# Performance work log

Measured on AMD Instinct MI355X. Metric: run time of the kernel, lower is better.

The kernel has to match this reference:

```python
import jax, jax.numpy as jnp
import numpy as np

B, S, D = 2, 2048, 1024
H, KV, HD = 16, 4, 64          # query heads, kv heads, head_dim
ROT = 32                        # partial rotary dim
G = H // KV                     # GQA group size
SCALE = HD ** -0.5


def _rotate_half(x):
    x1, x2 = x[..., : x.shape[-1] // 2], x[..., x.shape[-1] // 2 :]
    return jnp.concatenate((-x2, x1), axis=-1)


def setup_inputs() -> dict:
    key = jax.random.key(0)
    ks = jax.random.split(key, 8)
    hidden_states = jax.random.normal(ks[0], (B, S, D), dtype=jnp.float32)
    # real rotary tables: inv_freq over ROT//2 frequencies, duplicated halves
    inv_freq = 1.0 / (10000.0 ** (jnp.arange(0, ROT, 2, dtype=jnp.float32) / ROT))
    ang = jnp.arange(S, dtype=jnp.float32)[:, None] * inv_freq[None, :]  # [S, ROT/2]
    emb = jnp.concatenate([ang, ang], axis=-1)                           # [S, ROT]
    cos = jnp.broadcast_to(jnp.cos(emb)[None], (B, S, ROT))
    sin = jnp.broadcast_to(jnp.sin(emb)[None], (B, S, ROT))
    sd = lambda fan_in: 1.0 / np.sqrt(fan_in)
    q_w = jax.random.normal(ks[1], (D, H * HD), jnp.float32) * sd(D)
    q_b = jax.random.normal(ks[2], (H * HD,), jnp.float32) * 0.02
    k_w = jax.random.normal(ks[3], (D, KV * HD), jnp.float32) * sd(D)
    v_w = jax.random.normal(ks[4], (D, KV * HD), jnp.float32) * sd(D)
    v_b = jax.random.normal(ks[5], (KV * HD,), jnp.float32) * 0.02
    o_w = jax.random.normal(ks[6], (H * HD, D), jnp.float32) * sd(H * HD)
    o_b = jax.random.normal(ks[7], (D,), jnp.float32) * 0.02
    return {"hidden_states": hidden_states, "cos": cos, "sin": sin,
            "q_w": q_w, "q_b": q_b, "k_w": k_w, "v_w": v_w, "v_b": v_b,
            "o_w": o_w, "o_b": o_b}


def reference(hidden_states, cos, sin, q_w, q_b, k_w, v_w, v_b, o_w, o_b):
    x = hidden_states
    # projections -> [B, heads, S, HD]
    q = (x @ q_w + q_b).reshape(B, S, H, HD).transpose(0, 2, 1, 3)
    k = (x @ k_w).reshape(B, S, KV, HD).transpose(0, 2, 1, 3)
    v = (x @ v_w + v_b).reshape(B, S, KV, HD).transpose(0, 2, 1, 3)
    # partial RoPE; cos/sin broadcast over head dim
    c = cos[:, None, :, :]
    s = sin[:, None, :, :]
    q_rot, q_pass = q[..., :ROT], q[..., ROT:]
    k_rot, k_pass = k[..., :ROT], k[..., ROT:]
    q = jnp.concatenate([q_rot * c + _rotate_half(q_rot) * s, q_pass], axis=-1)
    k = jnp.concatenate([k_rot * c + _rotate_half(k_rot) * s, k_pass], axis=-1)
    # GQA without materializing repeated K/V: group queries per kv head
    qg = q.reshape(B, KV, G, S, HD)
    scores = jnp.einsum("bkgsd,bktd->bkgst", qg, k) * SCALE  # [B,KV,G,S,S]
    probs = jax.nn.softmax(scores, axis=-1)
    out = jnp.einsum("bkgst,bktd->bkgsd", probs, v)          # [B,KV,G,S,HD]
    out = out.reshape(B, H, S, HD).transpose(0, 2, 1, 3).reshape(B, S, H * HD)
    attn_output = out @ o_w + o_b
    attn_weights = probs.reshape(B, H, S, S)
    return attn_output, attn_weights
```

## Files before the change

### kernel.cpp

```cpp
#include <hip/hip_runtime.h>
#include <hip/hip_bf16.h>

typedef _Float16 f16;
typedef _Float16 f16x8 __attribute__((ext_vector_type(8)));
typedef _Float16 f16x4 __attribute__((ext_vector_type(4)));
typedef float f32x4 __attribute__((ext_vector_type(4)));

#define MFMA_F16(a, b, c) __builtin_amdgcn_mfma_f32_16x16x32_f16((a), (b), (c), 0, 0, 0)

static constexpr int S_TOK = 2048;
static constexpr int N_HEAD = 16;
static constexpr int N_KV = 4;
static constexpr int HD = 64;
static constexpr float SCL2E = 0.125f * 1.4426950408889634f;

static constexpr size_t OFF_X16 = 0;
static constexpr size_t OFF_QW = 4194304;
static constexpr size_t OFF_KW = OFF_QW + 1048576;
static constexpr size_t OFF_VW = OFF_KW + 262144;
static constexpr size_t OFF_OW = OFF_VW + 262144;
static constexpr size_t OFF_QS = OFF_OW + 1048576;
static constexpr size_t OFF_KS = OFF_QS + 4194304;
static constexpr size_t OFF_VS = OFF_KS + 1048576;
static constexpr size_t OFF_OS = OFF_VS + 1048576;
static constexpr size_t CVT_TOTAL = OFF_OW + 1048576;

__global__ __launch_bounds__(256) void k_cvt(
    const float* __restrict__ x, const float* __restrict__ qw,
    const float* __restrict__ kw, const float* __restrict__ vw,
    const float* __restrict__ ow, f16* __restrict__ dst) {
  size_t i = ((size_t)blockIdx.x * 256 + threadIdx.x) * 4;
  if (i >= CVT_TOTAL) return;
  const float* src;
  size_t off;
  if (i < OFF_QW) { src = x; off = i; }
  else if (i < OFF_KW) { src = qw; off = i - OFF_QW; }
  else if (i < OFF_VW) { src = kw; off = i - OFF_KW; }
  else if (i < OFF_OW) { src = vw; off = i - OFF_VW; }
  else { src = ow; off = i - OFF_OW; }
  float4 v = *(const float4*)(src + off);
  *(f16x4*)(dst + i) = f16x4{(f16)v.x, (f16)v.y, (f16)v.z, (f16)v.w};
}

__global__ __launch_bounds__(256) void k_qkv(
    const f16* __restrict__ x, const float* __restrict__ cosp,
    const float* __restrict__ sinp, const f16* __restrict__ q_w,
    const float* __restrict__ q_b, const f16* __restrict__ k_w,
    const f16* __restrict__ v_w, const float* __restrict__ v_b,
    f16* __restrict__ q_ws, f16* __restrict__ k_ws, f16* __restrict__ v_ws) {
  __shared__ f16 wb[64][72];
  const int tid = threadIdx.x;
  const int wave = tid >> 6, lane = tid & 63;
  const int l16 = lane & 15, g = lane >> 4;
  const int m0 = blockIdx.x * 64;
  const int n0 = blockIdx.y * 64;

  const f16* W;
  int ldW, nloc, mode;
  if (n0 < 1024) { W = q_w; ldW = 1024; nloc = n0; mode = 0; }
  else if (n0 < 1280) { W = k_w; ldW = 256; nloc = n0 - 1024; mode = 1; }
  else { W = v_w; ldW = 256; nloc = n0 - 1280; mode = 2; }

  f32x4 acc[4] = {};
  const int kk = (tid >> 4) * 4;
  const int nn = (tid & 15) * 4;

  for (int k0 = 0; k0 < 1024; k0 += 64) {
    const f16* wp = W + (size_t)(k0 + kk) * ldW + nloc + nn;
    f16x4 w0 = *(const f16x4*)(wp);
    f16x4 w1 = *(const f16x4*)(wp + ldW);
    f16x4 w2 = *(const f16x4*)(wp + 2 * ldW);
    f16x4 w3 = *(const f16x4*)(wp + 3 * ldW);
    __syncthreads();
    *(f16x4*)&wb[nn + 0][kk] = f16x4{w0[0], w1[0], w2[0], w3[0]};
    *(f16x4*)&wb[nn + 1][kk] = f16x4{w0[1], w1[1], w2[1], w3[1]};
    *(f16x4*)&wb[nn + 2][kk] = f16x4{w0[2], w1[2], w2[2], w3[2]};
    *(f16x4*)&wb[nn + 3][kk] = f16x4{w0[3], w1[3], w2[3], w3[3]};
    __syncthreads();
    const f16* xp = x + (size_t)(m0 + wave * 16 + l16) * 1024 + k0 + g * 8;
#pragma unroll
    for (int ks = 0; ks < 2; ++ks) {
      f16x8 af = *(const f16x8*)(xp + ks * 32);
#pragma unroll
      for (int n = 0; n < 4; ++n) {
        f16x8 bf = *(const f16x8*)&wb[n * 16 + l16][ks * 32 + g * 8];
        acc[n] = MFMA_F16(af, bf, acc[n]);
      }
    }
  }

  if (mode == 0) {
#pragma unroll
    for (int n = 0; n < 4; ++n) {
      float bsc = q_b[n0 + n * 16 + l16];
#pragma unroll
      for (int r = 0; r < 4; ++r) acc[n][r] += bsc;
    }
  } else if (mode == 2) {
#pragma unroll
    for (int n = 0; n < 4; ++n) {
      float bsc = v_b[nloc + n * 16 + l16];
#pragma unroll
      for (int r = 0; r < 4; ++r) acc[n][r] += bsc;
    }
  }
  if (mode < 2) {
#pragma unroll
    for (int r = 0; r < 4; ++r) {
      int row = m0 + wave * 16 + g * 4 + r;
      int bb = row >> 11, ss = row & 2047;
      float c = cosp[((size_t)bb * S_TOK + ss) * 32 + l16];
      float sn = sinp[((size_t)bb * S_TOK + ss) * 32 + l16];
      float v0 = acc[0][r], v1 = acc[1][r];
      acc[0][r] = v0 * c - v1 * sn;
      acc[1][r] = v1 * c + v0 * sn;
    }
  }
#pragma unroll
  for (int n = 0; n < 4; ++n) {
#pragma unroll
    for (int r = 0; r < 4; ++r) {
      int row = m0 + wave * 16 + g * 4 + r;
      int bb = row >> 11, ss = row & 2047;
      f16 val = (f16)acc[n][r];
      if (mode == 0) {
        int col = n0 + n * 16 + l16;
        int h = col >> 6, hd = col & 63;
        q_ws[(((size_t)bb * N_HEAD + h) * S_TOK + ss) * HD + hd] = val;
      } else {
        int col = nloc + n * 16 + l16;
        int kh = col >> 6, hd = col & 63;
        if (mode == 1)
          k_ws[(((size_t)bb * N_KV + kh) * S_TOK + ss) * HD + hd] = val;
        else
          v_ws[(((size_t)bb * N_KV + kh) * HD + hd) * S_TOK + ss] = val;
      }
    }
  }
}

__global__ __launch_bounds__(256, 3) void k_attn(
    const f16* __restrict__ q_ws, const f16* __restrict__ k_ws,
    const f16* __restrict__ v_ws, f16* __restrict__ o_ws,
    float* __restrict__ probs) {
  __shared__ f16 plds_all[4][32][72];
  __shared__ float lpart[2][2][32];
  __shared__ float osum[2][32][68];
  const int tid = threadIdx.x;
  const int wave = tid >> 6, lane = tid & 63;
  const int pairi = wave >> 1, half = wave & 1;
  const int l16 = lane & 15, g = lane >> 4;
  const int bid = blockIdx.x;
  const int combo = bid & 7, local = bid >> 3;
  const int b = combo >> 2, kvh = combo & 3;
  const int h = kvh * 4 + (local >> 5);
  const int rt = local & 31;
  const int head = b * N_HEAD + h;
  const int qrow0 = rt * 64 + pairi * 32;

  const f16* qb = q_ws + ((size_t)head * S_TOK + qrow0) * HD;
  const f16* kb = k_ws + (size_t)(b * N_KV + kvh) * S_TOK * HD;
  const f16* vb = v_ws + (size_t)(b * N_KV + kvh) * HD * S_TOK;
  float* pout = probs + (size_t)head * S_TOK * S_TOK + (size_t)qrow0 * S_TOK;
  f16(*plds)[72] = plds_all[wave];

  f16x8 qf[2][2];
#pragma unroll
  for (int mf = 0; mf < 2; ++mf)
#pragma unroll
    for (int ks = 0; ks < 2; ++ks)
      qf[mf][ks] = *(const f16x8*)(qb + (mf * 16 + l16) * HD + ks * 32 + g * 8);

  const int kt0 = half * 16, kt1 = kt0 + 16;

  float lsum[2][4] = {};
  for (int kt = kt0; kt < kt1; ++kt) {
    const f16* kp = kb + (size_t)kt * 64 * HD;
#pragma unroll
    for (int n = 0; n < 4; ++n) {
      f16x8 k0f = *(const f16x8*)(kp + (n * 16 + l16) * HD + g * 8);
      f16x8 k1f = *(const f16x8*)(kp + (n * 16 + l16) * HD + 32 + g * 8);
#pragma unroll
      for (int mf = 0; mf < 2; ++mf) {
        f32x4 s = {};
        s = MFMA_F16(qf[mf][0], k0f, s);
        s = MFMA_F16(qf[mf][1], k1f, s);
#pragma unroll
        for (int r = 0; r < 4; ++r) lsum[mf][r] += exp2f(s[r] * SCL2E);
      }
    }
  }
#pragma unroll
  for (int mf = 0; mf < 2; ++mf)
#pragma unroll
    for (int r = 0; r < 4; ++r) {
      float v = lsum[mf][r];
      v += __shfl_xor(v, 1, 64);
      v += __shfl_xor(v, 2, 64);
      v += __shfl_xor(v, 4, 64);
      v += __shfl_xor(v, 8, 64);
      lsum[mf][r] = v;
    }
  if (l16 == 0) {
#pragma unroll
    for (int mf = 0; mf < 2; ++mf)
#pragma unroll
      for (int r = 0; r < 4; ++r)
        lpart[pairi][half][mf * 16 + g * 4 + r] = lsum[mf][r];
  }
  __syncthreads();
  float linv[2][4];
#pragma unroll
  for (int mf = 0; mf < 2; ++mf)
#pragma unroll
    for (int r = 0; r < 4; ++r) {
      int row = mf * 16 + g * 4 + r;
      linv[mf][r] = 1.0f / (lpart[pairi][0][row] + lpart[pairi][1][row]);
    }

  f32x4 oacc[2][4] = {};
  const int orow = lane >> 4, oq = lane & 15;
  for (int kt = kt0; kt < kt1; ++kt) {
    const f16* kp = kb + (size_t)kt * 64 * HD;
#pragma unroll
    for (int n = 0; n < 4; ++n) {
      f16x8 k0f = *(const f16x8*)(kp + (n * 16 + l16) * HD + g * 8);
      f16x8 k1f = *(const f16x8*)(kp + (n * 16 + l16) * HD + 32 + g * 8);
#pragma unroll
      for (int mf = 0; mf < 2; ++mf) {
        f32x4 s = {};
        s = MFMA_F16(qf[mf][0], k0f, s);
        s = MFMA_F16(qf[mf][1], k1f, s);
#pragma unroll
        for (int r = 0; r < 4; ++r) {
          float p = exp2f(s[r] * SCL2E) * linv[mf][r];
          plds[mf * 16 + g * 4 + r][n * 16 + l16] = (f16)p;
        }
      }
    }
    asm volatile("s_waitcnt lgkmcnt(0)" ::: "memory");
    f16x8 pa[2][2];
#pragma unroll
    for (int mf = 0; mf < 2; ++mf)
#pragma unroll
      for (int ks = 0; ks < 2; ++ks)
        pa[mf][ks] = *(const f16x8*)&plds[mf * 16 + l16][ks * 32 + g * 8];
#pragma unroll
    for (int nh = 0; nh < 4; ++nh) {
      const f16* vp = vb + (size_t)(nh * 16 + l16) * S_TOK + kt * 64;
      f16x8 v0f = *(const f16x8*)(vp + g * 8);
      f16x8 v1f = *(const f16x8*)(vp + 32 + g * 8);
#pragma unroll
      for (int mf = 0; mf < 2; ++mf) {
        oacc[mf][nh] = MFMA_F16(pa[mf][0], v0f, oacc[mf][nh]);
        oacc[mf][nh] = MFMA_F16(pa[mf][1], v1f, oacc[mf][nh]);
      }
    }
#pragma unroll
    for (int it = 0; it < 8; ++it) {
      int rr = it * 4 + orow;
      f16x4 pv = *(const f16x4*)&plds[rr][oq * 4];
      f32x4 ov = {(float)pv[0], (float)pv[1], (float)pv[2], (float)pv[3]};
      __builtin_nontemporal_store(
          ov, (f32x4*)(pout + (size_t)rr * S_TOK + kt * 64 + oq * 4));
    }
    asm volatile("" ::: "memory");
  }

  if (half == 1) {
#pragma unroll
    for (int mf = 0; mf < 2; ++mf)
#pragma unroll
      for (int nh = 0; nh < 4; ++nh)
#pragma unroll
        for (int r = 0; r < 4; ++r)
          osum[pairi][mf * 16 + g * 4 + r][nh * 16 + l16] = oacc[mf][nh][r];
  }
  __syncthreads();
  if (half == 0) {
#pragma unroll
    for (int mf = 0; mf < 2; ++mf)
#pragma unroll
      for (int nh = 0; nh < 4; ++nh)
#pragma unroll
        for (int r = 0; r < 4; ++r) {
          int row = mf * 16 + g * 4 + r;
          float v = oacc[mf][nh][r] + osum[pairi][row][nh * 16 + l16];
          o_ws[((size_t)b * S_TOK + qrow0 + row) * 1024 + h * HD + nh * 16 +
               l16] = (f16)v;
        }
  }
}

__global__ __launch_bounds__(256) void k_oproj(
    const f16* __restrict__ a, const f16* __restrict__ o_w,
    const float* __restrict__ o_b, float* __restrict__ out) {
  __shared__ f16 wb[64][72];
  const int tid = threadIdx.x;
  const int wave = tid >> 6, lane = tid & 63;
  const int l16 = lane & 15, g = lane >> 4;
  const int m0 = blockIdx.x * 64, n0 = blockIdx.y * 64;
  f32x4 acc[4] = {};
  const int kk = (tid >> 4) * 4, nn = (tid & 15) * 4;
  for (int k0 = 0; k0 < 1024; k0 += 64) {
    const f16* wp = o_w + (size_t)(k0 + kk) * 1024 + n0 + nn;
    f16x4 w0 = *(const f16x4*)(wp);
    f16x4 w1 = *(const f16x4*)(wp + 1024);
    f16x4 w2 = *(const f16x4*)(wp + 2048);
    f16x4 w3 = *(const f16x4*)(wp + 3072);
    __syncthreads();
    *(f16x4*)&wb[nn + 0][kk] = f16x4{w0[0], w1[0], w2[0], w3[0]};
    *(f16x4*)&wb[nn + 1][kk] = f16x4{w0[1], w1[1], w2[1], w3[1]};
    *(f16x4*)&wb[nn + 2][kk] = f16x4{w0[2], w1[2], w2[2], w3[2]};
    *(f16x4*)&wb[nn + 3][kk] = f16x4{w0[3], w1[3], w2[3], w3[3]};
    __syncthreads();
    const f16* ap = a + (size_t)(m0 + wave * 16 + l16) * 1024 + k0 + g * 8;
#pragma unroll
    for (int ks = 0; ks < 2; ++ks) {
      f16x8 af = *(const f16x8*)(ap + ks * 32);
#pragma unroll
      for (int n = 0; n < 4; ++n) {
        f16x8 bf = *(const f16x8*)&wb[n * 16 + l16][ks * 32 + g * 8];
        acc[n] = MFMA_F16(af, bf, acc[n]);
      }
    }
  }
#pragma unroll
  for (int n = 0; n < 4; ++n) {
    float bsc = o_b[n0 + n * 16 + l16];
#pragma unroll
    for (int r = 0; r < 4; ++r) {
      int row = m0 + wave * 16 + g * 4 + r;
      out[(size_t)row * 1024 + n0 + n * 16 + l16] = acc[n][r] + bsc;
    }
  }
}

extern "C" void kernel_launch(void* const* d_in, const int* in_sizes, int n_in,
                              void* d_out, int out_size, void* d_ws,
                              size_t ws_size, hipStream_t stream) {
  (void)in_sizes; (void)n_in; (void)out_size; (void)ws_size;
  const float* x    = (const float*)d_in[0];
  const float* cosp = (const float*)d_in[1];
  const float* sinp = (const float*)d_in[2];
  const float* q_w  = (const float*)d_in[3];
  const float* q_b  = (const float*)d_in[4];
  const float* k_w  = (const float*)d_in[5];
  const float* v_w  = (const float*)d_in[6];
  const float* v_b  = (const float*)d_in[7];
  const float* o_w  = (const float*)d_in[8];
  const float* o_b  = (const float*)d_in[9];

  f16* ws = (f16*)d_ws;
  f16* x16  = ws + OFF_X16;
  f16* qw16 = ws + OFF_QW;
  f16* kw16 = ws + OFF_KW;
  f16* vw16 = ws + OFF_VW;
  f16* ow16 = ws + OFF_OW;
  f16* q_ws = ws + OFF_QS;
  f16* k_ws = ws + OFF_KS;
  f16* v_ws = ws + OFF_VS;
  f16* o_ws = ws + OFF_OS;
  float* out = (float*)d_out;
  float* probs = out + 4194304;

  k_cvt<<<dim3((CVT_TOTAL / 4 + 255) / 256), 256, 0, stream>>>(
      x, q_w, k_w, v_w, o_w, ws);
  k_qkv<<<dim3(64, 24), 256, 0, stream>>>(x16, cosp, sinp, qw16, q_b, kw16,
                                          vw16, v_b, q_ws, k_ws, v_ws);
  k_attn<<<dim3(1024), 256, 0, stream>>>(q_ws, k_ws, v_ws, o_ws, probs);
  k_oproj<<<dim3(64, 16), 256, 0, stream>>>(o_ws, ow16, o_b, out);
}
```

Measured before the change: 304.6 us.

## Split softmax row-sum pass into separate kernel writing partial sums to workspace

Moves the first pass of the two-pass attention (computing exp row sums over keys) out of k_attn into a new k_lsum kernel. k_lsum uses 2048 blocks with one 16-row tile per wave, and it stores two half-range partial sums per row in the x16 workspace region, which is no longer needed after the QKV projection. k_attn then reads the partial sums, drops its shared-memory reduction and __syncthreads, and computes only the normalized probabilities and PV. This aims for more parallelism and lower register pressure in each pass, at the cost of an extra kernel launch, a global round trip for the sums, and a second read of Q and K.

```diff
diff --git a/kernel.cpp b/kernel.cpp
--- a/kernel.cpp
+++ b/kernel.cpp
@@ -139,12 +139,54 @@
   }
 }
 
+__global__ __launch_bounds__(256) void k_lsum(
+    const f16* __restrict__ q_ws, const f16* __restrict__ k_ws,
+    float* __restrict__ lsum_ws) {
+  const int tid = threadIdx.x;
+  const int wave = tid >> 6, lane = tid & 63;
+  const int l16 = lane & 15, g = lane >> 4;
+  const int bid = blockIdx.x;
+  const int combo = bid & 7, local = bid >> 3;
+  const int b = combo >> 2, kvh = combo & 3;
+  const int hg = local >> 6;
+  const int rem = local & 63;
+  const int qt = rem >> 1, half = rem & 1;
+  const int head = b * N_HEAD + kvh * 4 + hg;
+  const int qrow0 = qt * 64 + wave * 16;
+
+  const f16* qb = q_ws + ((size_t)head * S_TOK + qrow0) * HD;
+  const f16* kb = k_ws + (size_t)(b * N_KV + kvh) * S_TOK * HD;
+
+  f16x8 qf[2];
+  qf[0] = *(const f16x8*)(qb + l16 * HD + g * 8);
+  qf[1] = *(const f16x8*)(qb + l16 * HD + 32 + g * 8);
+
+  float lsum = 0.0f;
+  const int kt0 = half * 16, kt1 = kt0 + 16;
+  for (int kt = kt0; kt < kt1; ++kt) {
+    const f16* kp = kb + (size_t)kt * 64 * HD;
+#pragma unroll
+    for (int n = 0; n < 4; ++n) {
+      f16x8 k0f = *(const f16x8*)(kp + (n * 16 + l16) * HD + g * 8);
+      f16x8 k1f = *(const f16x8*)(kp + (n * 16 + l16) * HD + 32 + g * 8);
+      f32x4 s = {};
+      s = MFMA_F16(k0f, qf[0], s);
+      s = MFMA_F16(k1f, qf[1], s);
+      lsum += exp2f(s[0] * SCL2E) + exp2f(s[1] * SCL2E) +
+              exp2f(s[2] * SCL2E) + exp2f(s[3] * SCL2E);
+    }
+  }
+  lsum += __shfl_xor(lsum, 16, 64);
+  lsum += __shfl_xor(lsum, 32, 64);
+  if (lane < 16)
+    lsum_ws[((size_t)head * S_TOK + qrow0 + l16) * 2 + half] = lsum;
+}
+
 __global__ __launch_bounds__(256, 3) void k_attn(
     const f16* __restrict__ q_ws, const f16* __restrict__ k_ws,
-    const f16* __restrict__ v_ws, f16* __restrict__ o_ws,
-    float* __restrict__ probs) {
+    const f16* __restrict__ v_ws, const float* __restrict__ lsum_ws,
+    f16* __restrict__ o_ws, float* __restrict__ probs) {
   __shared__ f16 plds_all[4][32][72];
-  __shared__ float lpart[2][2][32];
   __shared__ float osum[2][32][68];
   const int tid = threadIdx.x;
   const int wave = tid >> 6, lane = tid & 63;
@@ -171,52 +213,16 @@
     for (int ks = 0; ks < 2; ++ks)
       qf[mf][ks] = *(const f16x8*)(qb + (mf * 16 + l16) * HD + ks * 32 + g * 8);
 
+  float linv[2][4];
+#pragma unroll
+  for (int mf = 0; mf < 2; ++mf)
+#pragma unroll
+    for (int r = 0; r < 4; ++r) {
+      size_t base = ((size_t)head * S_TOK + qrow0 + mf * 16 + g * 4 + r) * 2;
+      linv[mf][r] = 1.0f / (lsum_ws[base] + lsum_ws[base + 1]);
+    }
+
   const int kt0 = half * 16, kt1 = kt0 + 16;
-
-  float lsum[2][4] = {};
-  for (int kt = kt0; kt < kt1; ++kt) {
-    const f16* kp = kb + (size_t)kt * 64 * HD;
-#pragma unroll
-    for (int n = 0; n < 4; ++n) {
-      f16x8 k0f = *(const f16x8*)(kp + (n * 16 + l16) * HD + g * 8);
-      f16x8 k1f = *(const f16x8*)(kp + (n * 16 + l16) * HD + 32 + g * 8);
-#pragma unroll
-      for (int mf = 0; mf < 2; ++mf) {
-        f32x4 s = {};
-        s = MFMA_F16(qf[mf][0], k0f, s);
-        s = MFMA_F16(qf[mf][1], k1f, s);
-#pragma unroll
-        for (int r = 0; r < 4; ++r) lsum[mf][r] += exp2f(s[r] * SCL2E);
-      }
-    }
-  }
-#pragma unroll
-  for (int mf = 0; mf < 2; ++mf)
-#pragma unroll
-    for (int r = 0; r < 4; ++r) {
-      float v = lsum[mf][r];
-      v += __shfl_xor(v, 1, 64);
-      v += __shfl_xor(v, 2, 64);
-      v += __shfl_xor(v, 4, 64);
-      v += __shfl_xor(v, 8, 64);
-      lsum[mf][r] = v;
-    }
-  if (l16 == 0) {
-#pragma unroll
-    for (int mf = 0; mf < 2; ++mf)
-#pragma unroll
-      for (int r = 0; r < 4; ++r)
-        lpart[pairi][half][mf * 16 + g * 4 + r] = lsum[mf][r];
-  }
-  __syncthreads();
-  float linv[2][4];
-#pragma unroll
-  for (int mf = 0; mf < 2; ++mf)
-#pragma unroll
-    for (int r = 0; r < 4; ++r) {
-      int row = mf * 16 + g * 4 + r;
-      linv[mf][r] = 1.0f / (lpart[pairi][0][row] + lpart[pairi][1][row]);
-    }
 
   f32x4 oacc[2][4] = {};
   const int orow = lane >> 4, oq = lane & 15;
@@ -361,6 +367,7 @@
   f16* k_ws = ws + OFF_KS;
   f16* v_ws = ws + OFF_VS;
   f16* o_ws = ws + OFF_OS;
+  float* lsum_ws = (float*)(ws + OFF_X16);
   float* out = (float*)d_out;
   float* probs = out + 4194304;
 
@@ -368,6 +375,8 @@
       x, q_w, k_w, v_w, o_w, ws);
   k_qkv<<<dim3(64, 24), 256, 0, stream>>>(x16, cosp, sinp, qw16, q_b, kw16,
                                           vw16, v_b, q_ws, k_ws, v_ws);
-  k_attn<<<dim3(1024), 256, 0, stream>>>(q_ws, k_ws, v_ws, o_ws, probs);
+  k_lsum<<<dim3(2048), 256, 0, stream>>>(q_ws, k_ws, lsum_ws);
+  k_attn<<<dim3(1024), 256, 0, stream>>>(q_ws, k_ws, v_ws, lsum_ws, o_ws,
+                                         probs);
   k_oproj<<<dim3(64, 16), 256, 0, stream>>>(o_ws, ow16, o_b, out);
 }
```

Measured after the change: 372.5 us. 22.3% more time.

## Use 128x128 LDS-tiled GEMMs with 2x2 wave layout for QKV and output projections

Applied to the files above, without the earlier changes.

The QKV and output-projection GEMMs now use 128x128 block tiles. Both the activation tile and the weight tile are staged in shared memory, and each wave computes a 64x64 sub-tile (4x4 MFMAs), where before A was read straight from global memory per wave. This raises arithmetic intensity and reuse of both operands, cutting global traffic per MFMA. In exchange there are fewer blocks (384 and 256), which may underfill the GPU's compute units, and register and LDS use per block goes up.

```diff
diff --git a/kernel.cpp b/kernel.cpp
--- a/kernel.cpp
+++ b/kernel.cpp
@@ -48,95 +48,127 @@
     const float* __restrict__ q_b, const f16* __restrict__ k_w,
     const f16* __restrict__ v_w, const float* __restrict__ v_b,
     f16* __restrict__ q_ws, f16* __restrict__ k_ws, f16* __restrict__ v_ws) {
-  __shared__ f16 wb[64][72];
+  __shared__ f16 at[128][72];
+  __shared__ f16 bt[128][72];
   const int tid = threadIdx.x;
   const int wave = tid >> 6, lane = tid & 63;
   const int l16 = lane & 15, g = lane >> 4;
-  const int m0 = blockIdx.x * 64;
-  const int n0 = blockIdx.y * 64;
+  const int wm = wave >> 1, wn = wave & 1;
+  const int m0 = blockIdx.x * 128;
+  const int n0 = blockIdx.y * 128;
 
   const f16* W;
-  int ldW, nloc, mode;
-  if (n0 < 1024) { W = q_w; ldW = 1024; nloc = n0; mode = 0; }
-  else if (n0 < 1280) { W = k_w; ldW = 256; nloc = n0 - 1024; mode = 1; }
-  else { W = v_w; ldW = 256; nloc = n0 - 1280; mode = 2; }
-
-  f32x4 acc[4] = {};
-  const int kk = (tid >> 4) * 4;
-  const int nn = (tid & 15) * 4;
+  int ldW, nbase;
+  if (n0 < 1024) { W = q_w; ldW = 1024; nbase = n0; }
+  else if (n0 < 1280) { W = k_w; ldW = 256; nbase = n0 - 1024; }
+  else { W = v_w; ldW = 256; nbase = n0 - 1280; }
+
+  f32x4 acc[4][4] = {};
+  const int arow = tid >> 3, asub = tid & 7;
+  const int bkr = (tid >> 4) * 4, bnc = (tid & 15) * 4;
 
   for (int k0 = 0; k0 < 1024; k0 += 64) {
-    const f16* wp = W + (size_t)(k0 + kk) * ldW + nloc + nn;
-    f16x4 w0 = *(const f16x4*)(wp);
-    f16x4 w1 = *(const f16x4*)(wp + ldW);
-    f16x4 w2 = *(const f16x4*)(wp + 2 * ldW);
-    f16x4 w3 = *(const f16x4*)(wp + 3 * ldW);
+    f16x8 av[4];
+#pragma unroll
+    for (int it = 0; it < 4; ++it)
+      av[it] = *(const f16x8*)(x + (size_t)(m0 + it * 32 + arow) * 1024 + k0 +
+                               asub * 8);
+    f16x4 bv[2][4];
+#pragma unroll
+    for (int it = 0; it < 2; ++it)
+#pragma unroll
+      for (int kk = 0; kk < 4; ++kk)
+        bv[it][kk] = *(const f16x4*)(W + (size_t)(k0 + bkr + kk) * ldW + nbase +
+                                     it * 64 + bnc);
     __syncthreads();
-    *(f16x4*)&wb[nn + 0][kk] = f16x4{w0[0], w1[0], w2[0], w3[0]};
-    *(f16x4*)&wb[nn + 1][kk] = f16x4{w0[1], w1[1], w2[1], w3[1]};
-    *(f16x4*)&wb[nn + 2][kk] = f16x4{w0[2], w1[2], w2[2], w3[2]};
-    *(f16x4*)&wb[nn + 3][kk] = f16x4{w0[3], w1[3], w2[3], w3[3]};
+#pragma unroll
+    for (int it = 0; it < 4; ++it)
+      *(f16x8*)&at[it * 32 + arow][asub * 8] = av[it];
+#pragma unroll
+    for (int it = 0; it < 2; ++it)
+#pragma unroll
+      for (int i = 0; i < 4; ++i)
+        *(f16x4*)&bt[it * 64 + bnc + i][bkr] =
+            f16x4{bv[it][0][i], bv[it][1][i], bv[it][2][i], bv[it][3][i]};
     __syncthreads();
-    const f16* xp = x + (size_t)(m0 + wave * 16 + l16) * 1024 + k0 + g * 8;
 #pragma unroll
     for (int ks = 0; ks < 2; ++ks) {
-      f16x8 af = *(const f16x8*)(xp + ks * 32);
-#pragma unroll
-      for (int n = 0; n < 4; ++n) {
-        f16x8 bf = *(const f16x8*)&wb[n * 16 + l16][ks * 32 + g * 8];
-        acc[n] = MFMA_F16(af, bf, acc[n]);
-      }
-    }
-  }
+      f16x8 af[4], bf[4];
+#pragma unroll
+      for (int mi = 0; mi < 4; ++mi)
+        af[mi] = *(const f16x8*)&at[wm * 64 + mi * 16 + l16][ks * 32 + g * 8];
+#pragma unroll
+      for (int ni = 0; ni < 4; ++ni)
+        bf[ni] = *(const f16x8*)&bt[wn * 64 + ni * 16 + l16][ks * 32 + g * 8];
+#pragma unroll
+      for (int mi = 0; mi < 4; ++mi)
+#pragma unroll
+        for (int ni = 0; ni < 4; ++ni)
+          acc[mi][ni] = MFMA_F16(af[mi], bf[ni], acc[mi][ni]);
+    }
+  }
+
+  const int gc0 = n0 + wn * 64;
+  int mode, nloc;
+  if (gc0 < 1024) { mode = 0; nloc = gc0; }
+  else if (gc0 < 1280) { mode = 1; nloc = gc0 - 1024; }
+  else { mode = 2; nloc = gc0 - 1280; }
 
   if (mode == 0) {
 #pragma unroll
-    for (int n = 0; n < 4; ++n) {
-      float bsc = q_b[n0 + n * 16 + l16];
-#pragma unroll
-      for (int r = 0; r < 4; ++r) acc[n][r] += bsc;
+    for (int ni = 0; ni < 4; ++ni) {
+      float bsc = q_b[gc0 + ni * 16 + l16];
+#pragma unroll
+      for (int mi = 0; mi < 4; ++mi)
+#pragma unroll
+        for (int r = 0; r < 4; ++r) acc[mi][ni][r] += bsc;
     }
   } else if (mode == 2) {
 #pragma unroll
-    for (int n = 0; n < 4; ++n) {
-      float bsc = v_b[nloc + n * 16 + l16];
-#pragma unroll
-      for (int r = 0; r < 4; ++r) acc[n][r] += bsc;
+    for (int ni = 0; ni < 4; ++ni) {
+      float bsc = v_b[nloc + ni * 16 + l16];
+#pragma unroll
+      for (int mi = 0; mi < 4; ++mi)
+#pragma unroll
+        for (int r = 0; r < 4; ++r) acc[mi][ni][r] += bsc;
     }
   }
   if (mode < 2) {
 #pragma unroll
-    for (int r = 0; r < 4; ++r) {
-      int row = m0 + wave * 16 + g * 4 + r;
-      int bb = row >> 11, ss = row & 2047;
-      float c = cosp[((size_t)bb * S_TOK + ss) * 32 + l16];
-      float sn = sinp[((size_t)bb * S_TOK + ss) * 32 + l16];
-      float v0 = acc[0][r], v1 = acc[1][r];
-      acc[0][r] = v0 * c - v1 * sn;
-      acc[1][r] = v1 * c + v0 * sn;
-    }
-  }
-#pragma unroll
-  for (int n = 0; n < 4; ++n) {
-#pragma unroll
-    for (int r = 0; r < 4; ++r) {
-      int row = m0 + wave * 16 + g * 4 + r;
-      int bb = row >> 11, ss = row & 2047;
-      f16 val = (f16)acc[n][r];
-      if (mode == 0) {
-        int col = n0 + n * 16 + l16;
-        int h = col >> 6, hd = col & 63;
-        q_ws[(((size_t)bb * N_HEAD + h) * S_TOK + ss) * HD + hd] = val;
-      } else {
-        int col = nloc + n * 16 + l16;
-        int kh = col >> 6, hd = col & 63;
-        if (mode == 1)
-          k_ws[(((size_t)bb * N_KV + kh) * S_TOK + ss) * HD + hd] = val;
-        else
-          v_ws[(((size_t)bb * N_KV + kh) * HD + hd) * S_TOK + ss] = val;
-      }
-    }
-  }
+    for (int mi = 0; mi < 4; ++mi)
+#pragma unroll
+      for (int r = 0; r < 4; ++r) {
+        int row = m0 + wm * 64 + mi * 16 + g * 4 + r;
+        int bb = row >> 11, ss = row & 2047;
+        float c = cosp[((size_t)bb * S_TOK + ss) * 32 + l16];
+        float sn = sinp[((size_t)bb * S_TOK + ss) * 32 + l16];
+        float v0 = acc[mi][0][r], v1 = acc[mi][1][r];
+        acc[mi][0][r] = v0 * c - v1 * sn;
+        acc[mi][1][r] = v1 * c + v0 * sn;
+      }
+  }
+#pragma unroll
+  for (int mi = 0; mi < 4; ++mi)
+#pragma unroll
+    for (int ni = 0; ni < 4; ++ni)
+#pragma unroll
+      for (int r = 0; r < 4; ++r) {
+        int row = m0 + wm * 64 + mi * 16 + g * 4 + r;
+        int bb = row >> 11, ss = row & 2047;
+        f16 val = (f16)acc[mi][ni][r];
+        if (mode == 0) {
+          int col = gc0 + ni * 16 + l16;
+          int h = col >> 6, hd = col & 63;
+          q_ws[(((size_t)bb * N_HEAD + h) * S_TOK + ss) * HD + hd] = val;
+        } else {
+          int col = nloc + ni * 16 + l16;
+          int kh = col >> 6, hd = col & 63;
+          if (mode == 1)
+            k_ws[(((size_t)bb * N_KV + kh) * S_TOK + ss) * HD + hd] = val;
+          else
+            v_ws[(((size_t)bb * N_KV + kh) * HD + hd) * S_TOK + ss] = val;
+        }
+      }
 }
 
 __global__ __launch_bounds__(256, 3) void k_attn(
@@ -295,44 +327,70 @@
 __global__ __launch_bounds__(256) void k_oproj(
     const f16* __restrict__ a, const f16* __restrict__ o_w,
     const float* __restrict__ o_b, float* __restrict__ out) {
-  __shared__ f16 wb[64][72];
+  __shared__ f16 at[128][72];
+  __shared__ f16 bt[128][72];
   const int tid = threadIdx.x;
   const int wave = tid >> 6, lane = tid & 63;
   const int l16 = lane & 15, g = lane >> 4;
-  const int m0 = blockIdx.x * 64, n0 = blockIdx.y * 64;
-  f32x4 acc[4] = {};
-  const int kk = (tid >> 4) * 4, nn = (tid & 15) * 4;
+  const int wm = wave >> 1, wn = wave & 1;
+  const int m0 = blockIdx.x * 128;
+  const int n0 = blockIdx.y * 128;
+
+  f32x4 acc[4][4] = {};
+  const int arow = tid >> 3, asub = tid & 7;
+  const int bkr = (tid >> 4) * 4, bnc = (tid & 15) * 4;
+
   for (int k0 = 0; k0 < 1024; k0 += 64) {
-    const f16* wp = o_w + (size_t)(k0 + kk) * 1024 + n0 + nn;
-    f16x4 w0 = *(const f16x4*)(wp);
-    f16x4 w1 = *(const f16x4*)(wp + 1024);
-    f16x4 w2 = *(const f16x4*)(wp + 2048);
-    f16x4 w3 = *(const f16x4*)(wp + 3072);
+    f16x8 av[4];
+#pragma unroll
+    for (int it = 0; it < 4; ++it)
+      av[it] = *(const f16x8*)(a + (size_t)(m0 + it * 32 + arow) * 1024 + k0 +
+                               asub * 8);
+    f16x4 bv[2][4];
+#pragma unroll
+    for (int it = 0; it < 2; ++it)
+#pragma unroll
+      for (int kk = 0; kk < 4; ++kk)
+        bv[it][kk] = *(const f16x4*)(o_w + (size_t)(k0 + bkr + kk) * 1024 + n0 +
+                                     it * 64 + bnc);
     __syncthreads();
-    *(f16x4*)&wb[nn + 0][kk] = f16x4{w0[0], w1[0], w2[0], w3[0]};
-    *(f16x4*)&wb[nn + 1][kk] = f16x4{w0[1], w1[1], w2[1], w3[1]};
-    *(f16x4*)&wb[nn + 2][kk] = f16x4{w0[2], w1[2], w2[2], w3[2]};
-    *(f16x4*)&wb[nn + 3][kk] = f16x4{w0[3], w1[3], w2[3], w3[3]};
+#pragma unroll
+    for (int it = 0; it < 4; ++it)
+      *(f16x8*)&at[it * 32 + arow][asub * 8] = av[it];
+#pragma unroll
+    for (int it = 0; it < 2; ++it)
+#pragma unroll
+      for (int i = 0; i < 4; ++i)
+        *(f16x4*)&bt[it * 64 + bnc + i][bkr] =
+            f16x4{bv[it][0][i], bv[it][1][i], bv[it][2][i], bv[it][3][i]};
     __syncthreads();
-    const f16* ap = a + (size_t)(m0 + wave * 16 + l16) * 1024 + k0 + g * 8;
 #pragma unroll
     for (int ks = 0; ks < 2; ++ks) {
-      f16x8 af = *(const f16x8*)(ap + ks * 32);
-#pragma unroll
-      for (int n = 0; n < 4; ++n) {
-        f16x8 bf = *(const f16x8*)&wb[n * 16 + l16][ks * 32 + g * 8];
-        acc[n] = MFMA_F16(af, bf, acc[n]);
-      }
-    }
-  }
-#pragma unroll
-  for (int n = 0; n < 4; ++n) {
-    float bsc = o_b[n0 + n * 16 + l16];
-#pragma unroll
-    for (int r = 0; r < 4; ++r) {
-      int row = m0 + wave * 16 + g * 4 + r;
-      out[(size_t)row * 1024 + n0 + n * 16 + l16] = acc[n][r] + bsc;
-    }
+      f16x8 af[4], bf[4];
+#pragma unroll
+      for (int mi = 0; mi < 4; ++mi)
+        af[mi] = *(const f16x8*)&at[wm * 64 + mi * 16 + l16][ks * 32 + g * 8];
+#pragma unroll
+      for (int ni = 0; ni < 4; ++ni)
+        bf[ni] = *(const f16x8*)&bt[wn * 64 + ni * 16 + l16][ks * 32 + g * 8];
+#pragma unroll
+      for (int mi = 0; mi < 4; ++mi)
+#pragma unroll
+        for (int ni = 0; ni < 4; ++ni)
+          acc[mi][ni] = MFMA_F16(af[mi], bf[ni], acc[mi][ni]);
+    }
+  }
+#pragma unroll
+  for (int ni = 0; ni < 4; ++ni) {
+    float bsc = o_b[n0 + wn * 64 + ni * 16 + l16];
+#pragma unroll
+    for (int mi = 0; mi < 4; ++mi)
+#pragma unroll
+      for (int r = 0; r < 4; ++r) {
+        int row = m0 + wm * 64 + mi * 16 + g * 4 + r;
+        out[(size_t)row * 1024 + n0 + wn * 64 + ni * 16 + l16] =
+            acc[mi][ni][r] + bsc;
+      }
   }
 }
 
@@ -366,8 +424,8 @@
 
   k_cvt<<<dim3((CVT_TOTAL / 4 + 255) / 256), 256, 0, stream>>>(
       x, q_w, k_w, v_w, o_w, ws);
-  k_qkv<<<dim3(64, 24), 256, 0, stream>>>(x16, cosp, sinp, qw16, q_b, kw16,
+  k_qkv<<<dim3(32, 12), 256, 0, stream>>>(x16, cosp, sinp, qw16, q_b, kw16,
                                           vw16, v_b, q_ws, k_ws, v_ws);
   k_attn<<<dim3(1024), 256, 0, stream>>>(q_ws, k_ws, v_ws, o_ws, probs);
-  k_oproj<<<dim3(64, 16), 256, 0, stream>>>(o_ws, ow16, o_b, out);
+  k_oproj<<<dim3(32, 8), 256, 0, stream>>>(o_ws, ow16, o_b, out);
 }
```

Measured after the change: 301.7 us. Within noise of the previous version (-0.9%).
